# Optimization experiments

Hardware: AMD Instinct MI355X
Metric: run time of the kernel (lower is better)

## Reference

```python
import jax, jax.numpy as jnp
import numpy as np

EPS = 1e-5

def _bn(t, gamma, beta):
    # training-mode BatchNorm2d: stats over (B,H,W), biased variance
    mean = jnp.mean(t, axis=(0, 2, 3), keepdims=True)
    var = jnp.var(t, axis=(0, 2, 3), keepdims=True)
    tn = (t - mean) * jax.lax.rsqrt(var + EPS)
    return tn * gamma[None, :, None, None] + beta[None, :, None, None]

def setup_inputs() -> dict:
    key = jax.random.key(0)
    ks = jax.random.split(key, 8)
    B, C, H, W = 16, 256, 64, 64
    u, k, v = 4, 16, 256
    s = 1.0 / np.sqrt(C)
    x = jax.random.normal(ks[0], (B, C, H, W), dtype=jnp.float32)
    Wq = jax.random.normal(ks[1], (k, C), dtype=jnp.float32) * s
    bq = jax.random.normal(ks[2], (k,), dtype=jnp.float32) * 0.01
    Wk = jax.random.normal(ks[3], (u * k, C), dtype=jnp.float32) * s
    bk = jax.random.normal(ks[4], (u * k,), dtype=jnp.float32) * 0.01
    Wv = jax.random.normal(ks[5], (u * v, C), dtype=jnp.float32) * s
    bv = jax.random.normal(ks[6], (u * v,), dtype=jnp.float32) * 0.01
    gamma_q = jnp.ones((k,), dtype=jnp.float32)
    beta_q = jnp.zeros((k,), dtype=jnp.float32)
    gamma_v = jnp.ones((u * v,), dtype=jnp.float32)
    beta_v = jnp.zeros((u * v,), dtype=jnp.float32)
    return {"x": x, "Wq": Wq, "bq": bq, "Wk": Wk, "bk": bk, "Wv": Wv, "bv": bv,
            "gamma_q": gamma_q, "beta_q": beta_q, "gamma_v": gamma_v, "beta_v": beta_v}

def reference(x, Wq, bq, Wk, bk, Wv, bv, gamma_q, beta_q, gamma_v, beta_v):
    B, C, H, W = x.shape
    k = Wq.shape[0]
    u = 4
    v = Wv.shape[0] // u
    # 1x1 convs as channel contractions
    Q = jnp.einsum('oc,bchw->bohw', Wq, x) + bq[None, :, None, None]   # [B,k,H,W]
    K = jnp.einsum('oc,bchw->bohw', Wk, x) + bk[None, :, None, None]   # [B,u*k,H,W]
    V = jnp.einsum('oc,bchw->bohw', Wv, x) + bv[None, :, None, None]   # [B,u*v,H,W]
    Q = _bn(Q, gamma_q, beta_q)
    V = _bn(V, gamma_v, beta_v)
    m = H * W
    Q = Q.reshape(B, k, m)          # [B,k,m]
    K = K.reshape(B, u, k, m)       # [B,u,k,m]
    V = V.reshape(B, u, v, m)       # [B,u,v,m]
    K = jax.nn.softmax(K, axis=3)
    context = jnp.einsum('bukm,buvm->bkv', K, V)   # [B,k,v]
    y = jnp.einsum('bkn,bkv->bvn', Q, context)     # [B,v,m]
    return y.reshape(B, v, H, W)
```

## Files before the change

### kernel.cpp

```cpp
#include <hip/hip_runtime.h>
#include <hip/hip_bf16.h>

typedef short s16x8 __attribute__((ext_vector_type(8)));
typedef short s16x4 __attribute__((ext_vector_type(4)));
typedef float f32x4 __attribute__((ext_vector_type(4)));
typedef unsigned u32;
typedef u32 u32x2 __attribute__((ext_vector_type(2)));

#define DI __device__ __forceinline__

constexpr int BB = 16;
constexpr int CC = 256;
constexpr int MM = 4096;
constexpr int KD = 16;
constexpr int UK = 64;
constexpr float EPSV = 1e-5f;

DI unsigned short f2bf(float f) {
  union { float f; unsigned u; } v; v.f = f;
  unsigned r = v.u + 0x7FFFu + ((v.u >> 16) & 1u);
  return (unsigned short)(r >> 16);
}
DI float bflo(u32 v) { union { u32 u; float f; } w; w.u = v << 16; return w.f; }
DI float bfhi(u32 v) { union { u32 u; float f; } w; w.u = v & 0xFFFF0000u; return w.f; }

__global__ __launch_bounds__(256) void k_cvt(const float* __restrict__ x,
    unsigned short* __restrict__ xbf, float* __restrict__ xsump) {
  int bid = blockIdx.x;
  size_t base = (size_t)bid * MM;
  int t = threadIdx.x;
  float s = 0.f;
#pragma unroll
  for (int i = 0; i < 4; ++i) {
    size_t idx = base + (size_t)(i * 256 + t) * 4;
    float4 v = *(const float4*)(x + idx);
    s16x4 c;
    c[0] = (short)f2bf(v.x); c[1] = (short)f2bf(v.y);
    c[2] = (short)f2bf(v.z); c[3] = (short)f2bf(v.w);
    *(s16x4*)&xbf[idx] = c;
    s += v.x + v.y + v.z + v.w;
  }
#pragma unroll
  for (int o = 32; o; o >>= 1) s += __shfl_down(s, o);
  __shared__ float red[4];
  if ((t & 63) == 0) red[t >> 6] = s;
  __syncthreads();
  if (t == 0) xsump[bid] = red[0] + red[1] + red[2] + red[3];
}

__global__ __launch_bounds__(512) void k_gxx(const unsigned short* __restrict__ xbf,
                                             u32* __restrict__ part) {
  int b = blockIdx.x >> 4, mc = blockIdx.x & 15;
  int m0 = mc * 256;
  __shared__ short lds[2][256 * 72];
  int t = threadIdx.x, w = t >> 6, l = t & 63;
  int wr = w >> 2, wc = w & 3;
  int lrow = l & 15, lk8 = (l >> 4) * 8;
  int srow = t >> 3, sseg = (t & 7) * 8;

  const unsigned short* gsrc = xbf + ((size_t)(b * CC + srow)) * MM + m0 + sseg;

  s16x8 rg[4];
#pragma unroll
  for (int i = 0; i < 4; ++i)
    rg[i] = *(const s16x8*)(gsrc + (size_t)i * 64 * MM);
#pragma unroll
  for (int i = 0; i < 4; ++i)
    *(s16x8*)&lds[0][(srow + i * 64) * 72 + sseg] = rg[i];

  f32x4 acc[8][4];
#pragma unroll
  for (int i = 0; i < 8; ++i)
#pragma unroll
    for (int j = 0; j < 4; ++j) acc[i][j] = (f32x4)0.f;

#pragma unroll
  for (int ks = 0; ks < 4; ++ks) {
    __syncthreads();
    if (ks < 3) {
#pragma unroll
      for (int i = 0; i < 4; ++i)
        rg[i] = *(const s16x8*)(gsrc + (size_t)i * 64 * MM + (ks + 1) * 64);
    }
    int buf = ks & 1;
#pragma unroll
    for (int half = 0; half < 2; ++half) {
      s16x8 af[8], bf[4];
#pragma unroll
      for (int i = 0; i < 8; ++i)
        af[i] = *(const s16x8*)&lds[buf][(wr * 128 + i * 16 + lrow) * 72 + half * 32 + lk8];
#pragma unroll
      for (int j = 0; j < 4; ++j)
        bf[j] = *(const s16x8*)&lds[buf][(wc * 64 + j * 16 + lrow) * 72 + half * 32 + lk8];
#pragma unroll
      for (int i = 0; i < 8; ++i)
#pragma unroll
        for (int j = 0; j < 4; ++j)
          acc[i][j] = __builtin_amdgcn_mfma_f32_16x16x32_bf16(af[i], bf[j], acc[i][j], 0, 0, 0);
    }
    if (ks < 3) {
#pragma unroll
      for (int i = 0; i < 4; ++i)
        *(s16x8*)&lds[buf ^ 1][(srow + i * 64) * 72 + sseg] = rg[i];
    }
  }

  size_t pb = (size_t)blockIdx.x * 32768;
#pragma unroll
  for (int i = 0; i < 8; ++i)
#pragma unroll
    for (int j = 0; j < 4; ++j) {
      int tau = (w * 8 + i) * 4 + j;
      u32x2 pk;
      pk[0] = (u32)f2bf(acc[i][j][0]) | ((u32)f2bf(acc[i][j][1]) << 16);
      pk[1] = (u32)f2bf(acc[i][j][2]) | ((u32)f2bf(acc[i][j][3]) << 16);
      *(u32x2*)&part[pb + tau * 128 + l * 2] = pk;
    }
}

__global__ __launch_bounds__(256) void k_gred(const u32* __restrict__ part,
                                              float* __restrict__ G) {
  int q = blockIdx.x * 256 + threadIdx.x;
  float s0 = 0.f, s1 = 0.f;
#pragma unroll 8
  for (int p = 0; p < 256; ++p) {
    u32 v = part[(size_t)p * 32768 + q];
    s0 += bflo(v);
    s1 += bfhi(v);
  }
  int r2 = q & 1, l = (q >> 1) & 63, tau = q >> 7;
  int j = tau & 3, i = (tau >> 2) & 7, w = tau >> 5;
  int wr = w >> 2, wc = w & 3;
  int row = wr * 128 + i * 16 + (l >> 4) * 4 + r2 * 2;
  int col = wc * 64 + j * 16 + (l & 15);
  G[row * 256 + col] = s0;
  G[(row + 1) * 256 + col] = s1;
}

__global__ __launch_bounds__(256) void k_proj(const unsigned short* __restrict__ xbf,
    const float* __restrict__ Wq, const float* __restrict__ bq,
    const float* __restrict__ Wk, const float* __restrict__ bk,
    float* __restrict__ Kb, float* __restrict__ Qb) {
  int b = blockIdx.x >> 5, mc = blockIdx.x & 31;
  int gm0 = mc * 128;
  __shared__ short wlds[80 * 264];
  __shared__ u32 xt[128 * 17];
  int t = threadIdx.x;
  int w = t >> 6, l = t & 63;
  int lrow = l & 15, lk = l >> 4;

#pragma unroll 4
  for (int o = 0; o < 80; ++o) {
    float v = (o < 64) ? Wk[o * CC + t] : Wq[(o - 64) * CC + t];
    wlds[o * 264 + t] = (short)f2bf(v);
  }

  f32x4 acc[5][2];
#pragma unroll
  for (int i = 0; i < 5; ++i) { acc[i][0] = (f32x4)0.f; acc[i][1] = (f32x4)0.f; }

  int c2 = t >> 4;
  int mq = t & 15;

  for (int ks = 0; ks < 8; ++ks) {
    int c0 = ks * 32;
    __syncthreads();
#pragma unroll
    for (int mb = 0; mb < 128; mb += 64) {
      int m = mb + mq * 4;
      const unsigned short* p0 = xbf + ((size_t)(b * CC + c0 + 2 * c2)) * MM + gm0 + m;
      s16x4 v0 = *(const s16x4*)p0;
      s16x4 v1 = *(const s16x4*)(p0 + MM);
      xt[(m + 0) * 17 + c2] = (u32)(unsigned short)v0[0] | ((u32)(unsigned short)v1[0] << 16);
      xt[(m + 1) * 17 + c2] = (u32)(unsigned short)v0[1] | ((u32)(unsigned short)v1[1] << 16);
      xt[(m + 2) * 17 + c2] = (u32)(unsigned short)v0[2] | ((u32)(unsigned short)v1[2] << 16);
      xt[(m + 3) * 17 + c2] = (u32)(unsigned short)v0[3] | ((u32)(unsigned short)v1[3] << 16);
    }
    __syncthreads();
    union { s16x8 v; u32 wd[4]; } bfr[2];
#pragma unroll
    for (int j = 0; j < 2; ++j) {
      int ml = w * 32 + j * 16 + lrow;
#pragma unroll
      for (int i = 0; i < 4; ++i) bfr[j].wd[i] = xt[ml * 17 + lk * 4 + i];
    }
#pragma unroll
    for (int ot = 0; ot < 5; ++ot) {
      s16x8 af = *(const s16x8*)&wlds[(ot * 16 + lrow) * 264 + c0 + lk * 8];
      acc[ot][0] = __builtin_amdgcn_mfma_f32_16x16x32_bf16(af, bfr[0].v, acc[ot][0], 0, 0, 0);
      acc[ot][1] = __builtin_amdgcn_mfma_f32_16x16x32_bf16(af, bfr[1].v, acc[ot][1], 0, 0, 0);
    }
  }

#pragma unroll
  for (int ot = 0; ot < 5; ++ot)
#pragma unroll
    for (int j = 0; j < 2; ++j)
#pragma unroll
      for (int r = 0; r < 4; ++r) {
        int o = ot * 16 + lk * 4 + r;
        int m = gm0 + w * 32 + j * 16 + lrow;
        float val = acc[ot][j][r];
        if (o < 64) Kb[((size_t)(b * UK + o)) * MM + m] = val + bk[o];
        else        Qb[((size_t)(b * KD + o - 64)) * MM + m] = val + bq[o - 64];
      }
}

__global__ __launch_bounds__(256) void k_sstats(const float* __restrict__ Kb,
    float* __restrict__ rmax, float* __restrict__ rsum) {
  int r = blockIdx.x;
  int t = threadIdx.x;
  const float4* p = (const float4*)(Kb + (size_t)r * MM);
  float4 v[4];
  float mx = -3.4e38f;
#pragma unroll
  for (int i = 0; i < 4; ++i) {
    v[i] = p[i * 256 + t];
    mx = fmaxf(mx, fmaxf(fmaxf(v[i].x, v[i].y), fmaxf(v[i].z, v[i].w)));
  }
#pragma unroll
  for (int o = 32; o; o >>= 1) mx = fmaxf(mx, __shfl_xor(mx, o));
  __shared__ float red[4];
  int w = t >> 6;
  if ((t & 63) == 0) red[w] = mx;
  __syncthreads();
  mx = fmaxf(fmaxf(red[0], red[1]), fmaxf(red[2], red[3]));
  float s = 0.f;
#pragma unroll
  for (int i = 0; i < 4; ++i)
    s += __expf(v[i].x - mx) + __expf(v[i].y - mx) +
         __expf(v[i].z - mx) + __expf(v[i].w - mx);
#pragma unroll
  for (int o = 32; o; o >>= 1) s += __shfl_xor(s, o);
  __syncthreads();
  if ((t & 63) == 0) red[w] = s;
  __syncthreads();
  if (t == 0) {
    rmax[r] = mx;
    rsum[r] = red[0] + red[1] + red[2] + red[3];
  }
}

__global__ __launch_bounds__(256) void k_fin(const float* __restrict__ G,
    const float* __restrict__ xsump,
    const float* __restrict__ Wv, const float* __restrict__ bv,
    const float* __restrict__ gv, const float* __restrict__ btv,
    const float* __restrict__ Wq, const float* __restrict__ bq,
    const float* __restrict__ gq, const float* __restrict__ btq,
    float* __restrict__ AV, float* __restrict__ BVa,
    float* __restrict__ AQ, float* __restrict__ BQa) {
  int t = threadIdx.x, w = t >> 6, l = t & 63;
  int o0 = blockIdx.x * 4;
  __shared__ float lw[4][256];
#pragma unroll
  for (int oo = 0; oo < 4; ++oo) {
    int o = o0 + oo;
    lw[oo][t] = (o < 1024) ? Wv[(size_t)o * CC + t] : Wq[(size_t)(o - 1024) * CC + t];
  }
  __syncthreads();

  float4 w4[4];
#pragma unroll
  for (int oo = 0; oo < 4; ++oo) w4[oo] = *(const float4*)&lw[oo][4 * l];

  float qf[4] = {0.f, 0.f, 0.f, 0.f};
#pragma unroll 4
  for (int i = 0; i < 64; ++i) {
    int r = i * 4 + w;
    float4 g4 = *(const float4*)(G + (size_t)r * CC + 4 * l);
#pragma unroll
    for (int oo = 0; oo < 4; ++oo) {
      float d = g4.x * w4[oo].x + g4.y * w4[oo].y + g4.z * w4[oo].z + g4.w * w4[oo].w;
      qf[oo] = fmaf(lw[oo][r], d, qf[oo]);
    }
  }

  float xs = 0.f;
#pragma unroll
  for (int bb = 0; bb < 16; ++bb) xs += xsump[bb * 256 + t];
  float sx[4];
#pragma unroll
  for (int oo = 0; oo < 4; ++oo) sx[oo] = lw[oo][t] * xs;

#pragma unroll
  for (int oo = 0; oo < 4; ++oo)
#pragma unroll
    for (int od = 32; od; od >>= 1) {
      qf[oo] += __shfl_xor(qf[oo], od);
      sx[oo] += __shfl_xor(sx[oo], od);
    }
  __shared__ float rq[4][4], rs[4][4];
  if (l == 0)
#pragma unroll
    for (int oo = 0; oo < 4; ++oo) { rq[w][oo] = qf[oo]; rs[w][oo] = sx[oo]; }
  __syncthreads();
  if (t < 4) {
    int oo = t, o = o0 + oo;
    float q = rq[0][oo] + rq[1][oo] + rq[2][oo] + rq[3][oo];
    float s = rs[0][oo] + rs[1][oo] + rs[2][oo] + rs[3][oo];
    float bias, gamma, beta; float *pa, *pb;
    if (o < 1024) { bias = bv[o]; gamma = gv[o]; beta = btv[o]; pa = AV + o; pb = BVa + o; }
    else { int oi = o - 1024; bias = bq[oi]; gamma = gq[oi]; beta = btq[oi]; pa = AQ + oi; pb = BQa + oi; }
    const float invN = 1.f / 65536.f;
    float mean = s * invN + bias;
    float e2 = q * invN + 2.f * bias * s * invN + bias * bias;
    float var = e2 - mean * mean;
    float a = gamma * rsqrtf(var + EPSV);
    *pa = a;
    *pb = beta - mean * a;
  }
}

__global__ __launch_bounds__(256) void k_xp(const unsigned short* __restrict__ xbf,
    const float* __restrict__ Kb, const float* __restrict__ rmax,
    float* __restrict__ xpp) {
  int b = blockIdx.x >> 4, kc = blockIdx.x & 15;
  int kbase = kc * 256;
  __shared__ short la[64][40];
  __shared__ short lb[256][40];
  int t = threadIdx.x, w = t >> 6, l = t & 63;
  int lrow = l & 15, lk = (l >> 4) * 8;

  f32x4 acc[4][4];
#pragma unroll
  for (int i = 0; i < 4; ++i)
#pragma unroll
    for (int j = 0; j < 4; ++j) acc[i][j] = (f32x4)0.f;

  for (int ks = 0; ks < 8; ++ks) {
    int k0 = kbase + ks * 32;
    __syncthreads();
    {
      int r = t >> 2, sg = (t & 3) * 8;
      const float4* src = (const float4*)(Kb + ((size_t)(b * UK + r)) * MM + k0 + sg);
      float rm = rmax[b * UK + r];
      s16x8 wv;
#pragma unroll
      for (int i = 0; i < 2; ++i) {
        float4 v = src[i];
        wv[i * 4 + 0] = (short)f2bf(__expf(v.x - rm));
        wv[i * 4 + 1] = (short)f2bf(__expf(v.y - rm));
        wv[i * 4 + 2] = (short)f2bf(__expf(v.z - rm));
        wv[i * 4 + 3] = (short)f2bf(__expf(v.w - rm));
      }
      *(s16x8*)&la[r][sg] = wv;
    }
#pragma unroll
    for (int i = 0; i < 4; ++i) {
      int r = i * 64 + (t >> 2), sg = (t & 3) * 8;
      s16x8 v = *(const s16x8*)&xbf[((size_t)(b * CC + r)) * MM + k0 + sg];
      *(s16x8*)&lb[r][sg] = v;
    }
    __syncthreads();
    s16x8 af[4], bfr[4];
#pragma unroll
    for (int i = 0; i < 4; ++i) af[i] = *(const s16x8*)&la[i * 16 + lrow][lk];
#pragma unroll
    for (int j = 0; j < 4; ++j) bfr[j] = *(const s16x8*)&lb[w * 64 + j * 16 + lrow][lk];
#pragma unroll
    for (int i = 0; i < 4; ++i)
#pragma unroll
      for (int j = 0; j < 4; ++j)
        acc[i][j] = __builtin_amdgcn_mfma_f32_16x16x32_bf16(af[i], bfr[j], acc[i][j], 0, 0, 0);
  }
  float* dst = xpp + (size_t)blockIdx.x * UK * CC;
#pragma unroll
  for (int i = 0; i < 4; ++i)
#pragma unroll
    for (int j = 0; j < 4; ++j)
#pragma unroll
      for (int r = 0; r < 4; ++r) {
        int row = i * 16 + (l >> 4) * 4 + r;
        int col = w * 64 + j * 16 + lrow;
        dst[row * 256 + col] = acc[i][j][r];
      }
}

__global__ __launch_bounds__(256) void k_ctx(const float* __restrict__ xpp,
    const float* __restrict__ rsum,
    const float* __restrict__ Wv, const float* __restrict__ bv,
    const float* __restrict__ AV, const float* __restrict__ BVa,
    float* __restrict__ CTX) {
  int b = blockIdx.x >> 4, kk = blockIdx.x & 15;
  __shared__ float lxp[4][256];
  int t = threadIdx.x;
#pragma unroll
  for (int u = 0; u < 4; ++u) {
    int row = u * KD + kk;
    float s = 0.f;
#pragma unroll
    for (int kc = 0; kc < 16; ++kc)
      s += xpp[((size_t)(b * 16 + kc) * UK + row) * CC + t];
    lxp[u][t] = s / rsum[b * UK + row];
  }
  __syncthreads();
  float acc = 0.f;
#pragma unroll
  for (int u = 0; u < 4; ++u) {
    int ch = u * 256 + t;
    const float4* wv4 = (const float4*)(Wv + (size_t)ch * CC);
    float dot = 0.f;
#pragma unroll 8
    for (int c4 = 0; c4 < 64; ++c4) {
      float4 wv = wv4[c4];
      dot += wv.x * lxp[u][c4 * 4 + 0] + wv.y * lxp[u][c4 * 4 + 1] +
             wv.z * lxp[u][c4 * 4 + 2] + wv.w * lxp[u][c4 * 4 + 3];
    }
    acc += AV[ch] * (dot + bv[ch]) + BVa[ch];
  }
  CTX[((size_t)b * KD + kk) * 256 + t] = acc;
}

__global__ __launch_bounds__(256) void k_y(const float* __restrict__ Qb,
    const float* __restrict__ CTX,
    const float* __restrict__ AQ, const float* __restrict__ BQa,
    float* __restrict__ y) {
  int b = blockIdx.x >> 4, nc = blockIdx.x & 15;
  int m = nc * 256 + threadIdx.x;
  float qn[16];
#pragma unroll
  for (int kk = 0; kk < 16; ++kk)
    qn[kk] = AQ[kk] * Qb[((size_t)b * KD + kk) * MM + m] + BQa[kk];
  const float* cb = CTX + (size_t)b * KD * 256;
  float* yo = y + (size_t)b * 256 * MM + m;
#pragma unroll 4
  for (int vv = 0; vv < 256; ++vv) {
    float acc = 0.f;
#pragma unroll
    for (int kk = 0; kk < 16; ++kk)
      acc = fmaf(qn[kk], cb[kk * 256 + vv], acc);
    yo[(size_t)vv * MM] = acc;
  }
}

extern "C" void kernel_launch(void* const* d_in, const int* in_sizes, int n_in,
                              void* d_out, int out_size, void* d_ws, size_t ws_size,
                              hipStream_t stream) {
  const float* x   = (const float*)d_in[0];
  const float* Wq  = (const float*)d_in[1];
  const float* bq  = (const float*)d_in[2];
  const float* Wk  = (const float*)d_in[3];
  const float* bk  = (const float*)d_in[4];
  const float* Wv  = (const float*)d_in[5];
  const float* bv  = (const float*)d_in[6];
  const float* gq  = (const float*)d_in[7];
  const float* btq = (const float*)d_in[8];
  const float* gv  = (const float*)d_in[9];
  const float* btv = (const float*)d_in[10];
  float* out = (float*)d_out;
  float* ws  = (float*)d_ws;

  float* G     = ws;
  float* XSUMP = ws + 65536;
  float* RMAX  = ws + 69632;
  float* RSUM  = ws + 70656;
  float* AV    = ws + 71680;
  float* BVa   = ws + 72704;
  float* AQ    = ws + 73728;
  float* BQa   = ws + 73744;
  float* CTX   = ws + 73984;
  float* XPP   = ws + 139520;
  float* KB    = ws + 4333824;
  float* QB    = ws + 8528128;
  u32*  PART   = (u32*)(ws + 139520);
  unsigned short* XBF = (unsigned short*)(ws + 9576704);

  k_cvt   <<<4096, 256, 0, stream>>>(x, XBF, XSUMP);
  k_gxx   <<<256,  512, 0, stream>>>(XBF, PART);
  k_gred  <<<128,  256, 0, stream>>>(PART, G);
  k_proj  <<<512,  256, 0, stream>>>(XBF, Wq, bq, Wk, bk, KB, QB);
  k_sstats<<<1024, 256, 0, stream>>>(KB, RMAX, RSUM);
  k_fin   <<<260,  256, 0, stream>>>(G, XSUMP, Wv, bv, gv, btv, Wq, bq, gq, btq,
                                     AV, BVa, AQ, BQa);
  k_xp    <<<256,  256, 0, stream>>>(XBF, KB, RMAX, XPP);
  k_ctx   <<<256,  256, 0, stream>>>(XPP, RSUM, Wv, bv, AV, BVa, CTX);
  k_y     <<<256,  256, 0, stream>>>(QB, CTX, AQ, BQa, out);
}
```

Measured before the change: 161.2 us.

## Split context kernel into bf16 prep and MFMA GEMM for Wv projection

Replaces the scalar k_ctx kernel, where each thread ran a 256-wide fp32 dot product against Wv rows, with three kernels. One reduces and normalises the softmax-weighted partial sums into bf16, one pre-scales Wv by the BN scale into bf16, and a small MFMA GEMM (64 blocks of 64 threads) computes the context matrix plus the bias constants. This targets the serial FP32 FMA work and the repeated Wv reads, at the cost of two extra launches, bf16 rounding of the operands, and a very small grid for the GEMM.

```diff
diff --git a/kernel.cpp b/kernel.cpp
--- a/kernel.cpp
+++ b/kernel.cpp
@@ -376,39 +376,82 @@
       }
 }
 
-__global__ __launch_bounds__(256) void k_ctx(const float* __restrict__ xpp,
-    const float* __restrict__ rsum,
-    const float* __restrict__ Wv, const float* __restrict__ bv,
-    const float* __restrict__ AV, const float* __restrict__ BVa,
-    float* __restrict__ CTX) {
+__global__ __launch_bounds__(256) void k_xpn(const float* __restrict__ xpp,
+    const float* __restrict__ rsum, unsigned short* __restrict__ xpn) {
   int b = blockIdx.x >> 4, kk = blockIdx.x & 15;
-  __shared__ float lxp[4][256];
   int t = threadIdx.x;
+  unsigned short* dst = xpn + ((size_t)(b * 16 + kk)) * 1024;
 #pragma unroll
   for (int u = 0; u < 4; ++u) {
-    int row = u * KD + kk;
+    int row = u * 16 + kk;
     float s = 0.f;
 #pragma unroll
     for (int kc = 0; kc < 16; ++kc)
       s += xpp[((size_t)(b * 16 + kc) * UK + row) * CC + t];
-    lxp[u][t] = s / rsum[b * UK + row];
-  }
-  __syncthreads();
-  float acc = 0.f;
-#pragma unroll
-  for (int u = 0; u < 4; ++u) {
-    int ch = u * 256 + t;
-    const float4* wv4 = (const float4*)(Wv + (size_t)ch * CC);
-    float dot = 0.f;
-#pragma unroll 8
-    for (int c4 = 0; c4 < 64; ++c4) {
-      float4 wv = wv4[c4];
-      dot += wv.x * lxp[u][c4 * 4 + 0] + wv.y * lxp[u][c4 * 4 + 1] +
-             wv.z * lxp[u][c4 * 4 + 2] + wv.w * lxp[u][c4 * 4 + 3];
-    }
-    acc += AV[ch] * (dot + bv[ch]) + BVa[ch];
-  }
-  CTX[((size_t)b * KD + kk) * 256 + t] = acc;
+    s /= rsum[b * UK + row];
+    dst[u * 256 + t] = f2bf(s);
+  }
+}
+
+__global__ __launch_bounds__(256) void k_wvs(const float* __restrict__ Wv,
+    const float* __restrict__ AV, unsigned short* __restrict__ wvs) {
+  int ch = blockIdx.x;
+  int t = threadIdx.x;
+  float a = AV[ch];
+  wvs[(size_t)ch * CC + t] = f2bf(a * Wv[(size_t)ch * CC + t]);
+}
+
+__global__ __launch_bounds__(64) void k_ctx2(const unsigned short* __restrict__ xpn,
+    const unsigned short* __restrict__ wvs,
+    const float* __restrict__ AV, const float* __restrict__ bv,
+    const float* __restrict__ BVa, float* __restrict__ CTX) {
+  int mt = blockIdx.x >> 3, nt = blockIdx.x & 7;
+  int m0 = mt * 32, n0 = nt * 32;
+  int l = threadIdx.x;
+  int lrow = l & 15, lk8 = (l >> 4) * 8;
+
+  f32x4 acc[2][2];
+#pragma unroll
+  for (int i = 0; i < 2; ++i)
+#pragma unroll
+    for (int j = 0; j < 2; ++j) acc[i][j] = (f32x4)0.f;
+
+#pragma unroll 4
+  for (int k0 = 0; k0 < 1024; k0 += 32) {
+    int u = k0 >> 8, c0 = k0 & 255;
+    s16x8 a0 = *(const s16x8*)&xpn[(size_t)(m0 + lrow) * 1024 + k0 + lk8];
+    s16x8 a1 = *(const s16x8*)&xpn[(size_t)(m0 + 16 + lrow) * 1024 + k0 + lk8];
+    s16x8 b0 = *(const s16x8*)&wvs[(size_t)(u * 256 + n0 + lrow) * CC + c0 + lk8];
+    s16x8 b1 = *(const s16x8*)&wvs[(size_t)(u * 256 + n0 + 16 + lrow) * CC + c0 + lk8];
+    acc[0][0] = __builtin_amdgcn_mfma_f32_16x16x32_bf16(a0, b0, acc[0][0], 0, 0, 0);
+    acc[0][1] = __builtin_amdgcn_mfma_f32_16x16x32_bf16(a0, b1, acc[0][1], 0, 0, 0);
+    acc[1][0] = __builtin_amdgcn_mfma_f32_16x16x32_bf16(a1, b0, acc[1][0], 0, 0, 0);
+    acc[1][1] = __builtin_amdgcn_mfma_f32_16x16x32_bf16(a1, b1, acc[1][1], 0, 0, 0);
+  }
+
+  float cst[2];
+#pragma unroll
+  for (int j = 0; j < 2; ++j) {
+    int vv = n0 + j * 16 + lrow;
+    float s = 0.f;
+#pragma unroll
+    for (int u = 0; u < 4; ++u) {
+      int ch = u * 256 + vv;
+      s += AV[ch] * bv[ch] + BVa[ch];
+    }
+    cst[j] = s;
+  }
+
+#pragma unroll
+  for (int i = 0; i < 2; ++i)
+#pragma unroll
+    for (int j = 0; j < 2; ++j)
+#pragma unroll
+      for (int r = 0; r < 4; ++r) {
+        int row = m0 + i * 16 + (l >> 4) * 4 + r;
+        int col = n0 + j * 16 + lrow;
+        CTX[(size_t)row * 256 + col] = acc[i][j][r] + cst[j];
+      }
 }
 
 __global__ __launch_bounds__(256) void k_y(const float* __restrict__ Qb,
@@ -464,6 +507,8 @@
   float* QB    = ws + 8528128;
   u32*  PART   = (u32*)(ws + 139520);
   unsigned short* XBF = (unsigned short*)(ws + 9576704);
+  unsigned short* XPN = (unsigned short*)(ws + 17965312);
+  unsigned short* WVS = (unsigned short*)(ws + 18096384);
 
   k_cvt   <<<4096, 256, 0, stream>>>(x, XBF, XSUMP);
   k_gxx   <<<256,  512, 0, stream>>>(XBF, PART);
@@ -473,6 +518,8 @@
   k_fin   <<<260,  256, 0, stream>>>(G, XSUMP, Wv, bv, gv, btv, Wq, bq, gq, btq,
                                      AV, BVa, AQ, BQa);
   k_xp    <<<256,  256, 0, stream>>>(XBF, KB, RMAX, XPP);
-  k_ctx   <<<256,  256, 0, stream>>>(XPP, RSUM, Wv, bv, AV, BVa, CTX);
+  k_xpn   <<<256,  256, 0, stream>>>(XPP, RSUM, XPN);
+  k_wvs   <<<1024, 256, 0, stream>>>(Wv, AV, WVS);
+  k_ctx2  <<<64,   64,  0, stream>>>(XPN, WVS, AV, bv, BVa, CTX);
   k_y     <<<256,  256, 0, stream>>>(QB, CTX, AQ, BQa, out);
 }
```

Result: faster. 145.5 us (-9.7%).
